# Kernel tuning notes

Hardware: AMD Instinct MI355X
Metric: run time of the kernel (lower is better)

The kernel has to match this reference:

```python
import jax, jax.numpy as jnp
import numpy as np

INPUT = 256
HIDDEN = 1024
OUTPUT = 256
B, T = 64, 512


def setup_inputs() -> dict:
    key = jax.random.key(0)
    ks = jax.random.split(key, 7)
    s_ih = 1.0 / np.sqrt(INPUT)
    s_hh = 1.0 / np.sqrt(HIDDEN)
    return {
        "input_seq": jax.random.normal(ks[0], (B, T, INPUT), jnp.float32),
        "W_ih": jax.random.uniform(ks[1], (INPUT, 4 * HIDDEN), jnp.float32, -s_ih, s_ih),
        "W_hh": jax.random.uniform(ks[2], (HIDDEN, 4 * HIDDEN), jnp.float32, -s_hh, s_hh),
        "b_ih": jax.random.uniform(ks[3], (4 * HIDDEN,), jnp.float32, -s_hh, s_hh),
        "b_hh": jax.random.uniform(ks[4], (4 * HIDDEN,), jnp.float32, -s_hh, s_hh),
        "W_out": jax.random.uniform(ks[5], (HIDDEN, OUTPUT), jnp.float32, -s_hh, s_hh),
        "b_out": jax.random.uniform(ks[6], (OUTPUT,), jnp.float32, -s_hh, s_hh),
    }


def _lstm_last_hidden(x, W_ih, W_hh, b_ih, b_hh):
    Bsz = x.shape[0]
    H = W_hh.shape[0]
    # Precompute input-side gate projections for all timesteps: [T, B, 4H]
    x_t = jnp.einsum('bti,ih->tbh', x, W_ih) + b_ih + b_hh

    def step(carry, xg):
        h, c = carry
        gates = xg + h @ W_hh  # [B, 4H]
        i, f, g, o = jnp.split(gates, 4, axis=-1)
        i = jax.nn.sigmoid(i)
        f = jax.nn.sigmoid(f)
        g = jnp.tanh(g)
        o = jax.nn.sigmoid(o)
        c = f * c + i * g
        h = o * jnp.tanh(c)
        return (h, c), None

    h0 = jnp.zeros((Bsz, H), x.dtype)
    c0 = jnp.zeros((Bsz, H), x.dtype)
    (h_last, _), _ = jax.lax.scan(step, (h0, c0), x_t)
    return h_last


def reference(input_seq, W_ih, W_hh, b_ih, b_hh, W_out, b_out):
    h_last = _lstm_last_hidden(input_seq, W_ih, W_hh, b_ih, b_hh)  # [B, H]
    return h_last @ W_out + b_out  # [B, OUTPUT]
```

## Files before the change

### kernel.cpp

```cpp
#include <hip/hip_runtime.h>
#include <hip/hip_bf16.h>
#include <cstdint>

#define HIDDEN 1024
#define INPUT  256
#define BATCH  64
#define TSTEPS 512
#define NGCOL  4096
#define KTOT   1280
#define HBUFN  65536

typedef __attribute__((ext_vector_type(8))) short bf16x8;
typedef __attribute__((ext_vector_type(4))) float f32x4;
typedef unsigned long long u64;
typedef unsigned int u32;

__device__ inline short f2bs(float f) {
    union { __hip_bfloat16 h; short s; } u;
    u.h = __float2bfloat16(f);
    return u.s;
}
__device__ inline unsigned short f2bu(float f) {
    union { __hip_bfloat16 h; unsigned short s; } u;
    u.h = __float2bfloat16(f);
    return u.s;
}

__global__ __launch_bounds__(256) void build_wt(
    const float* __restrict__ Whh, const float* __restrict__ Wih,
    __hip_bfloat16* __restrict__ Wt)
{
    int t = blockIdx.x * 256 + threadIdx.x;
    int col = t & 4095;
    int k0  = (t >> 12) * 16;
    __hip_bfloat16 tmp[16];
    if (k0 < HIDDEN) {
        #pragma unroll
        for (int i = 0; i < 16; ++i)
            tmp[i] = __float2bfloat16(Whh[(size_t)(k0 + i) * NGCOL + col]);
    } else {
        #pragma unroll
        for (int i = 0; i < 16; ++i)
            tmp[i] = __float2bfloat16(Wih[(size_t)(k0 - HIDDEN + i) * NGCOL + col]);
    }
    #pragma unroll
    for (int i = 0; i < 16; ++i)
        Wt[(size_t)col * KTOT + k0 + i] = tmp[i];
}

__global__ __launch_bounds__(256) void init_state(
    const float* __restrict__ bih, const float* __restrict__ bhh,
    float* __restrict__ bias, u32* __restrict__ hbuf)
{
    int i = blockIdx.x * 256 + threadIdx.x;
    if (i < NGCOL) bias[i] = bih[i] + bhh[i];
    hbuf[i] = 0u;
}

__global__ __launch_bounds__(512, 2) void lstm_persist(
    const __hip_bfloat16* __restrict__ Wt,
    const float* __restrict__ x,
    u32* __restrict__ hbuf,
    float* __restrict__ hf,
    const float* __restrict__ bias)
{
    __shared__ float pbuf[8][1025];

    const int tid  = threadIdx.x;
    const int wg   = blockIdx.x;
    const int bg   = wg >> 6;
    const int cg   = wg & 63;
    const int wave = tid >> 6;
    const int lane = tid & 63;
    const int l15  = lane & 15;
    const int l4   = lane >> 4;
    const int b0   = bg * 16;
    const int n0   = cg * 16;

    const __hip_bfloat16* wrow = Wt + (size_t)(n0 + l15) * KTOT;
    bf16x8 w[5][4];
    #pragma unroll
    for (int c5 = 0; c5 < 5; ++c5) {
        const int kk = (wave + c5 * 8) * 32 + l4 * 8;
        #pragma unroll
        for (int g = 0; g < 4; ++g)
            w[c5][g] = *(const bf16x8*)(wrow + (size_t)g * 1024 * KTOT + kk);
    }

    const int br = tid >> 4;
    const int hc = tid & 15;
    float creg = 0.f;
    float bi = 0.f, bfr = 0.f, bgg = 0.f, bo = 0.f;
    if (tid < 256) {
        bi  = bias[0 * 1024 + n0 + hc];
        bfr = bias[1 * 1024 + n0 + hc];
        bgg = bias[2 * 1024 + n0 + hc];
        bo  = bias[3 * 1024 + n0 + hc];
    }

    const int hoff = (b0 + l15) * HIDDEN + wave * 32 + l4 * 8;
    const float* xrow = x + ((size_t)(b0 + l15) * TSTEPS) * INPUT + wave * 32 + l4 * 8;

    for (int t = 0; t < TSTEPS; ++t) {
        const u32* hb = hbuf + (t & 1) * HBUFN;
        u32*       ho = hbuf + ((t + 1) & 1) * HBUFN;

        bf16x8 afx;
        {
            const float* xf = xrow + (size_t)t * INPUT;
            float4 pa = *(const float4*)(xf);
            float4 pb = *(const float4*)(xf + 4);
            afx[0] = f2bs(pa.x); afx[1] = f2bs(pa.y); afx[2] = f2bs(pa.z); afx[3] = f2bs(pa.w);
            afx[4] = f2bs(pb.x); afx[5] = f2bs(pb.y); afx[6] = f2bs(pb.z); afx[7] = f2bs(pb.w);
        }

        u64 hq[4][4];
        {
            const u64 want = ((u64)(u32)t << 16) | ((u64)(u32)t << 48);
            const u64 mask = 0xFFFF0000FFFF0000ull;
            for (;;) {
                u64 bad = 0;
                #pragma unroll
                for (int c5 = 0; c5 < 4; ++c5) {
                    const u64* hp = (const u64*)(hb + hoff + c5 * 256);
                    #pragma unroll
                    for (int q = 0; q < 4; ++q) {
                        hq[c5][q] = __hip_atomic_load(hp + q, __ATOMIC_RELAXED,
                                                      __HIP_MEMORY_SCOPE_AGENT);
                        bad |= (hq[c5][q] ^ want) & mask;
                    }
                }
                if (__all(bad == 0)) break;
                __builtin_amdgcn_s_sleep(1);
            }
        }
        bf16x8 afh[4];
        #pragma unroll
        for (int c5 = 0; c5 < 4; ++c5) {
            union { u32 p[4]; bf16x8 v; } u;
            #pragma unroll
            for (int q = 0; q < 4; ++q) {
                const u64 d = hq[c5][q];
                u.p[q] = (u32)(d & 0xFFFFu) | ((u32)(d >> 32) << 16);
            }
            afh[c5] = u.v;
        }

        f32x4 a0 = {0.f, 0.f, 0.f, 0.f};
        f32x4 a1 = a0, a2 = a0, a3 = a0;
        #pragma unroll
        for (int c5 = 0; c5 < 4; ++c5) {
            a0 = __builtin_amdgcn_mfma_f32_16x16x32_bf16(afh[c5], w[c5][0], a0, 0, 0, 0);
            a1 = __builtin_amdgcn_mfma_f32_16x16x32_bf16(afh[c5], w[c5][1], a1, 0, 0, 0);
            a2 = __builtin_amdgcn_mfma_f32_16x16x32_bf16(afh[c5], w[c5][2], a2, 0, 0, 0);
            a3 = __builtin_amdgcn_mfma_f32_16x16x32_bf16(afh[c5], w[c5][3], a3, 0, 0, 0);
        }
        a0 = __builtin_amdgcn_mfma_f32_16x16x32_bf16(afx, w[4][0], a0, 0, 0, 0);
        a1 = __builtin_amdgcn_mfma_f32_16x16x32_bf16(afx, w[4][1], a1, 0, 0, 0);
        a2 = __builtin_amdgcn_mfma_f32_16x16x32_bf16(afx, w[4][2], a2, 0, 0, 0);
        a3 = __builtin_amdgcn_mfma_f32_16x16x32_bf16(afx, w[4][3], a3, 0, 0, 0);

        #pragma unroll
        for (int c5 = 0; c5 < 5; ++c5)
            #pragma unroll
            for (int g = 0; g < 4; ++g)
                asm volatile("" : "+v"(w[c5][g]));

        float* pw = &pbuf[wave][0];
        #pragma unroll
        for (int r = 0; r < 4; ++r) {
            const int row = l4 * 4 + r;
            pw[(0 * 16 + row) * 16 + l15] = a0[r];
            pw[(1 * 16 + row) * 16 + l15] = a1[r];
            pw[(2 * 16 + row) * 16 + l15] = a2[r];
            pw[(3 * 16 + row) * 16 + l15] = a3[r];
        }
        __syncthreads();

        if (tid < 256) {
            float gi = bi, gf = bfr, gg = bgg, go = bo;
            #pragma unroll
            for (int w8 = 0; w8 < 8; ++w8) {
                const float* p = &pbuf[w8][0];
                gi += p[(0 * 16 + br) * 16 + hc];
                gf += p[(1 * 16 + br) * 16 + hc];
                gg += p[(2 * 16 + br) * 16 + hc];
                go += p[(3 * 16 + br) * 16 + hc];
            }
            const float i_ = 1.f / (1.f + __expf(-gi));
            const float f_ = 1.f / (1.f + __expf(-gf));
            const float g_ = tanhf(gg);
            const float o_ = 1.f / (1.f + __expf(-go));
            creg = f_ * creg + i_ * g_;
            const float h = o_ * tanhf(creg);
            if (t == TSTEPS - 1) {
                hf[(b0 + br) * HIDDEN + n0 + hc] = h;
            } else {
                const u32 val = ((u32)(t + 1) << 16) | (u32)f2bu(h);
                __hip_atomic_store(ho + (b0 + br) * HIDDEN + n0 + hc, val,
                                   __ATOMIC_RELAXED, __HIP_MEMORY_SCOPE_AGENT);
            }
        }
        if (t == TSTEPS - 1) break;
        __syncthreads();
    }
}

__global__ __launch_bounds__(256) void out_proj(
    const float* __restrict__ hf, const float* __restrict__ Wout,
    const float* __restrict__ bout, float* __restrict__ out)
{
    const int b  = blockIdx.x;
    const int oc = threadIdx.x;
    const float* hb = hf + (size_t)b * HIDDEN;
    float a0 = 0.f, a1 = 0.f, a2 = 0.f, a3 = 0.f;
    for (int k = 0; k < HIDDEN; k += 4) {
        a0 += hb[k + 0] * Wout[(size_t)(k + 0) * 256 + oc];
        a1 += hb[k + 1] * Wout[(size_t)(k + 1) * 256 + oc];
        a2 += hb[k + 2] * Wout[(size_t)(k + 2) * 256 + oc];
        a3 += hb[k + 3] * Wout[(size_t)(k + 3) * 256 + oc];
    }
    out[b * 256 + oc] = (a0 + a1) + (a2 + a3) + bout[oc];
}

extern "C" void kernel_launch(void* const* d_in, const int* in_sizes, int n_in,
                              void* d_out, int out_size, void* d_ws, size_t ws_size,
                              hipStream_t stream)
{
    const float* x    = (const float*)d_in[0];
    const float* Wih  = (const float*)d_in[1];
    const float* Whh  = (const float*)d_in[2];
    const float* bih  = (const float*)d_in[3];
    const float* bhh  = (const float*)d_in[4];
    const float* Wout = (const float*)d_in[5];
    const float* bout = (const float*)d_in[6];
    float* out = (float*)d_out;

    char* ws = (char*)d_ws;
    size_t off = 0;
    auto alloc = [&](size_t bytes) -> void* {
        void* p = ws + off;
        off = (off + bytes + 255) & ~(size_t)255;
        return p;
    };
    __hip_bfloat16* Wt = (__hip_bfloat16*)alloc((size_t)NGCOL * KTOT * 2);
    u32*   hbuf = (u32*)alloc((size_t)2 * HBUFN * 4);
    float* bias = (float*)alloc((size_t)NGCOL * 4);
    float* hf   = (float*)alloc((size_t)BATCH * HIDDEN * 4);

    build_wt<<<1280, 256, 0, stream>>>(Whh, Wih, Wt);
    init_state<<<512, 256, 0, stream>>>(bih, bhh, bias, hbuf);
    lstm_persist<<<256, 512, 0, stream>>>(Wt, x, hbuf, hf, bias);
    out_proj<<<64, 256, 0, stream>>>(hf, Wout, bout, out);
}
```

Before: 2.984 ms.

## Double-buffer LDS partials, hoist x-MFMA before spin, per-element polling

Double-buffers the per-wave partial-sum LDS array by timestep parity, so the second per-step barrier can be removed and only one raw s_barrier with an lgkmcnt wait remains. The input-projection MFMAs are moved ahead of the wait on the hidden state so they overlap the spin. The whole-wave retry loop with sleep is replaced by issuing all loads once and then re-polling each stale element individually. The aim is to shorten the serial per-step critical path, at the cost of doubled LDS use and busier polling with no sleep. The asm register pins on the weights are also dropped, which risks the compiler spilling or rematerialising them.

```diff
diff --git a/kernel.cpp b/kernel.cpp
--- a/kernel.cpp
+++ b/kernel.cpp
@@ -64,7 +64,7 @@
     float* __restrict__ hf,
     const float* __restrict__ bias)
 {
-    __shared__ float pbuf[8][1025];
+    __shared__ float pbuf[2][8][1025];
 
     const int tid  = threadIdx.x;
     const int wg   = blockIdx.x;
@@ -113,25 +113,32 @@
             afx[0] = f2bs(pa.x); afx[1] = f2bs(pa.y); afx[2] = f2bs(pa.z); afx[3] = f2bs(pa.w);
             afx[4] = f2bs(pb.x); afx[5] = f2bs(pb.y); afx[6] = f2bs(pb.z); afx[7] = f2bs(pb.w);
         }
-
+        f32x4 a0 = {0.f, 0.f, 0.f, 0.f};
+        f32x4 a1 = a0, a2 = a0, a3 = a0;
+        a0 = __builtin_amdgcn_mfma_f32_16x16x32_bf16(afx, w[4][0], a0, 0, 0, 0);
+        a1 = __builtin_amdgcn_mfma_f32_16x16x32_bf16(afx, w[4][1], a1, 0, 0, 0);
+        a2 = __builtin_amdgcn_mfma_f32_16x16x32_bf16(afx, w[4][2], a2, 0, 0, 0);
+        a3 = __builtin_amdgcn_mfma_f32_16x16x32_bf16(afx, w[4][3], a3, 0, 0, 0);
+
+        const u64 want = ((u64)(u32)t << 16) | ((u64)(u32)t << 48);
+        const u64 emask = 0xFFFF0000FFFF0000ull;
         u64 hq[4][4];
-        {
-            const u64 want = ((u64)(u32)t << 16) | ((u64)(u32)t << 48);
-            const u64 mask = 0xFFFF0000FFFF0000ull;
-            for (;;) {
-                u64 bad = 0;
-                #pragma unroll
-                for (int c5 = 0; c5 < 4; ++c5) {
-                    const u64* hp = (const u64*)(hb + hoff + c5 * 256);
-                    #pragma unroll
-                    for (int q = 0; q < 4; ++q) {
-                        hq[c5][q] = __hip_atomic_load(hp + q, __ATOMIC_RELAXED,
-                                                      __HIP_MEMORY_SCOPE_AGENT);
-                        bad |= (hq[c5][q] ^ want) & mask;
-                    }
-                }
-                if (__all(bad == 0)) break;
-                __builtin_amdgcn_s_sleep(1);
+        #pragma unroll
+        for (int c5 = 0; c5 < 4; ++c5) {
+            const u64* hp = (const u64*)(hb + hoff + c5 * 256);
+            #pragma unroll
+            for (int q = 0; q < 4; ++q)
+                hq[c5][q] = __hip_atomic_load(hp + q, __ATOMIC_RELAXED,
+                                              __HIP_MEMORY_SCOPE_AGENT);
+        }
+        #pragma unroll
+        for (int c5 = 0; c5 < 4; ++c5) {
+            const u64* hp = (const u64*)(hb + hoff + c5 * 256);
+            #pragma unroll
+            for (int q = 0; q < 4; ++q) {
+                while (((hq[c5][q] ^ want) & emask) != 0ull)
+                    hq[c5][q] = __hip_atomic_load(hp + q, __ATOMIC_RELAXED,
+                                                  __HIP_MEMORY_SCOPE_AGENT);
             }
         }
         bf16x8 afh[4];
@@ -146,8 +153,6 @@
             afh[c5] = u.v;
         }
 
-        f32x4 a0 = {0.f, 0.f, 0.f, 0.f};
-        f32x4 a1 = a0, a2 = a0, a3 = a0;
         #pragma unroll
         for (int c5 = 0; c5 < 4; ++c5) {
             a0 = __builtin_amdgcn_mfma_f32_16x16x32_bf16(afh[c5], w[c5][0], a0, 0, 0, 0);
@@ -155,18 +160,8 @@
             a2 = __builtin_amdgcn_mfma_f32_16x16x32_bf16(afh[c5], w[c5][2], a2, 0, 0, 0);
             a3 = __builtin_amdgcn_mfma_f32_16x16x32_bf16(afh[c5], w[c5][3], a3, 0, 0, 0);
         }
-        a0 = __builtin_amdgcn_mfma_f32_16x16x32_bf16(afx, w[4][0], a0, 0, 0, 0);
-        a1 = __builtin_amdgcn_mfma_f32_16x16x32_bf16(afx, w[4][1], a1, 0, 0, 0);
-        a2 = __builtin_amdgcn_mfma_f32_16x16x32_bf16(afx, w[4][2], a2, 0, 0, 0);
-        a3 = __builtin_amdgcn_mfma_f32_16x16x32_bf16(afx, w[4][3], a3, 0, 0, 0);
-
-        #pragma unroll
-        for (int c5 = 0; c5 < 5; ++c5)
-            #pragma unroll
-            for (int g = 0; g < 4; ++g)
-                asm volatile("" : "+v"(w[c5][g]));
-
-        float* pw = &pbuf[wave][0];
+
+        float* pw = &pbuf[t & 1][wave][0];
         #pragma unroll
         for (int r = 0; r < 4; ++r) {
             const int row = l4 * 4 + r;
@@ -175,13 +170,17 @@
             pw[(2 * 16 + row) * 16 + l15] = a2[r];
             pw[(3 * 16 + row) * 16 + l15] = a3[r];
         }
-        __syncthreads();
+
+        __builtin_amdgcn_sched_barrier(0);
+        asm volatile("s_waitcnt lgkmcnt(0)" ::: "memory");
+        __builtin_amdgcn_s_barrier();
+        __builtin_amdgcn_sched_barrier(0);
 
         if (tid < 256) {
             float gi = bi, gf = bfr, gg = bgg, go = bo;
             #pragma unroll
             for (int w8 = 0; w8 < 8; ++w8) {
-                const float* p = &pbuf[w8][0];
+                const float* p = &pbuf[t & 1][w8][0];
                 gi += p[(0 * 16 + br) * 16 + hc];
                 gf += p[(1 * 16 + br) * 16 + hc];
                 gg += p[(2 * 16 + br) * 16 + hc];
@@ -201,8 +200,6 @@
                                    __ATOMIC_RELAXED, __HIP_MEMORY_SCOPE_AGENT);
             }
         }
-        if (t == TSTEPS - 1) break;
-        __syncthreads();
     }
 }
 
```

New measurement: 4.193 ms. 1.41x slower.

## Stage hidden state per XCD so blocks poll XCD-local copies instead of global

Applied to the files above, without the earlier changes.

Blocks learn their XCC ID and rank through a global counter handshake. At each timestep, the waves of each XCD cooperatively copy the validated previous hidden state from the global double buffer into a per-XCD staging buffer. Each block then polls that staging copy with volatile loads, falling back to direct agent-scope atomic polling after many tries. The input-projection MFMAs are moved ahead of the wait to overlap with it. The aim is to cut cross-XCD coherent polling traffic, at the cost of an extra copy per step, a startup barrier, and reliance on volatile loads being coherent within an XCD's L2.

```diff
diff --git a/kernel.cpp b/kernel.cpp
--- a/kernel.cpp
+++ b/kernel.cpp
@@ -9,6 +9,8 @@
 #define NGCOL  4096
 #define KTOT   1280
 #define HBUFN  65536
+#define STAGEN 65536
+#define NXCD   8
 
 typedef __attribute__((ext_vector_type(8))) short bf16x8;
 typedef __attribute__((ext_vector_type(4))) float f32x4;
@@ -50,21 +52,27 @@
 
 __global__ __launch_bounds__(256) void init_state(
     const float* __restrict__ bih, const float* __restrict__ bhh,
-    float* __restrict__ bias, u32* __restrict__ hbuf)
+    float* __restrict__ bias, u32* __restrict__ hbuf,
+    u32* __restrict__ staging, u32* __restrict__ cnt)
 {
     int i = blockIdx.x * 256 + threadIdx.x;
     if (i < NGCOL) bias[i] = bih[i] + bhh[i];
-    hbuf[i] = 0u;
+    if (i < 2 * HBUFN) hbuf[i] = 0u;
+    staging[i] = 0u;
+    if (i < 256) cnt[i] = 0u;
 }
 
 __global__ __launch_bounds__(512, 2) void lstm_persist(
     const __hip_bfloat16* __restrict__ Wt,
     const float* __restrict__ x,
     u32* __restrict__ hbuf,
+    u32* __restrict__ staging,
     float* __restrict__ hf,
-    const float* __restrict__ bias)
+    const float* __restrict__ bias,
+    u32* __restrict__ cnt)
 {
     __shared__ float pbuf[8][1025];
+    __shared__ u32 pro[3];
 
     const int tid  = threadIdx.x;
     const int wg   = blockIdx.x;
@@ -77,6 +85,26 @@
     const int b0   = bg * 16;
     const int n0   = cg * 16;
 
+    if (tid == 0) {
+        u32 xcc;
+        asm volatile("s_getreg_b32 %0, hwreg(HW_REG_XCC_ID)" : "=s"(xcc));
+        xcc &= 7u;
+        u32 rank = __hip_atomic_fetch_add(cnt + xcc * 16, 1u,
+                                          __ATOMIC_RELAXED, __HIP_MEMORY_SCOPE_AGENT);
+        __hip_atomic_fetch_add(cnt + 8 * 16, 1u,
+                               __ATOMIC_RELAXED, __HIP_MEMORY_SCOPE_AGENT);
+        while (__hip_atomic_load(cnt + 8 * 16, __ATOMIC_RELAXED,
+                                 __HIP_MEMORY_SCOPE_AGENT) < 256u)
+            __builtin_amdgcn_s_sleep(2);
+        u32 nx = __hip_atomic_load(cnt + xcc * 16, __ATOMIC_RELAXED,
+                                   __HIP_MEMORY_SCOPE_AGENT);
+        pro[0] = xcc; pro[1] = rank; pro[2] = nx;
+    }
+    __syncthreads();
+    const u32 myxcd = pro[0];
+    const u32 nw    = pro[2] * 8u;
+    const u32 rw    = pro[1] * 8u + (u32)wave;
+
     const __hip_bfloat16* wrow = Wt + (size_t)(n0 + l15) * KTOT;
     bf16x8 w[5][4];
     #pragma unroll
@@ -104,34 +132,72 @@
     for (int t = 0; t < TSTEPS; ++t) {
         const u32* hb = hbuf + (t & 1) * HBUFN;
         u32*       ho = hbuf + ((t + 1) & 1) * HBUFN;
+        u32*       sg = staging + ((size_t)myxcd * 2 + (t & 1)) * STAGEN;
+
+        const u64 want  = ((u64)(u32)t << 16) | ((u64)(u32)t << 48);
+        const u64 emask = 0xFFFF0000FFFF0000ull;
+
+        const float* xf = xrow + (size_t)t * INPUT;
+        float4 pa = *(const float4*)(xf);
+        float4 pb = *(const float4*)(xf + 4);
+
+        for (u32 s = rw; s < 256u; s += nw) {
+            const u32 off = (s >> 2) * 1024u + (s & 3u) * 256u + (u32)lane * 4u;
+            const u64* sp = (const u64*)(hb + off);
+            u64 d0, d1;
+            for (;;) {
+                d0 = __hip_atomic_load(sp,     __ATOMIC_RELAXED, __HIP_MEMORY_SCOPE_AGENT);
+                d1 = __hip_atomic_load(sp + 1, __ATOMIC_RELAXED, __HIP_MEMORY_SCOPE_AGENT);
+                if (__all((((d0 ^ want) | (d1 ^ want)) & emask) == 0ull)) break;
+                __builtin_amdgcn_s_sleep(1);
+            }
+            u64* dp = (u64*)(sg + off);
+            dp[0] = d0; dp[1] = d1;
+        }
 
         bf16x8 afx;
-        {
-            const float* xf = xrow + (size_t)t * INPUT;
-            float4 pa = *(const float4*)(xf);
-            float4 pb = *(const float4*)(xf + 4);
-            afx[0] = f2bs(pa.x); afx[1] = f2bs(pa.y); afx[2] = f2bs(pa.z); afx[3] = f2bs(pa.w);
-            afx[4] = f2bs(pb.x); afx[5] = f2bs(pb.y); afx[6] = f2bs(pb.z); afx[7] = f2bs(pb.w);
-        }
+        afx[0] = f2bs(pa.x); afx[1] = f2bs(pa.y); afx[2] = f2bs(pa.z); afx[3] = f2bs(pa.w);
+        afx[4] = f2bs(pb.x); afx[5] = f2bs(pb.y); afx[6] = f2bs(pb.z); afx[7] = f2bs(pb.w);
+        f32x4 a0 = {0.f, 0.f, 0.f, 0.f};
+        f32x4 a1 = a0, a2 = a0, a3 = a0;
+        a0 = __builtin_amdgcn_mfma_f32_16x16x32_bf16(afx, w[4][0], a0, 0, 0, 0);
+        a1 = __builtin_amdgcn_mfma_f32_16x16x32_bf16(afx, w[4][1], a1, 0, 0, 0);
+        a2 = __builtin_amdgcn_mfma_f32_16x16x32_bf16(afx, w[4][2], a2, 0, 0, 0);
+        a3 = __builtin_amdgcn_mfma_f32_16x16x32_bf16(afx, w[4][3], a3, 0, 0, 0);
 
         u64 hq[4][4];
         {
-            const u64 want = ((u64)(u32)t << 16) | ((u64)(u32)t << 48);
-            const u64 mask = 0xFFFF0000FFFF0000ull;
-            for (;;) {
+            int tries = 0; bool ok = false;
+            while (!ok) {
                 u64 bad = 0;
                 #pragma unroll
                 for (int c5 = 0; c5 < 4; ++c5) {
-                    const u64* hp = (const u64*)(hb + hoff + c5 * 256);
+                    volatile const u64* vp = (volatile const u64*)(sg + hoff + c5 * 256);
                     #pragma unroll
                     for (int q = 0; q < 4; ++q) {
-                        hq[c5][q] = __hip_atomic_load(hp + q, __ATOMIC_RELAXED,
-                                                      __HIP_MEMORY_SCOPE_AGENT);
-                        bad |= (hq[c5][q] ^ want) & mask;
+                        hq[c5][q] = vp[q];
+                        bad |= (hq[c5][q] ^ want) & emask;
                     }
                 }
-                if (__all(bad == 0)) break;
-                __builtin_amdgcn_s_sleep(1);
+                ok = __all(bad == 0);
+                if (!ok && ++tries > 2048) break;
+            }
+            if (!ok) {
+                for (;;) {
+                    u64 bad = 0;
+                    #pragma unroll
+                    for (int c5 = 0; c5 < 4; ++c5) {
+                        const u64* hp = (const u64*)(hb + hoff + c5 * 256);
+                        #pragma unroll
+                        for (int q = 0; q < 4; ++q) {
+                            hq[c5][q] = __hip_atomic_load(hp + q, __ATOMIC_RELAXED,
+                                                          __HIP_MEMORY_SCOPE_AGENT);
+                            bad |= (hq[c5][q] ^ want) & emask;
+                        }
+                    }
+                    if (__all(bad == 0)) break;
+                    __builtin_amdgcn_s_sleep(1);
+                }
             }
         }
         bf16x8 afh[4];
@@ -146,8 +212,6 @@
             afh[c5] = u.v;
         }
 
-        f32x4 a0 = {0.f, 0.f, 0.f, 0.f};
-        f32x4 a1 = a0, a2 = a0, a3 = a0;
         #pragma unroll
         for (int c5 = 0; c5 < 4; ++c5) {
             a0 = __builtin_amdgcn_mfma_f32_16x16x32_bf16(afh[c5], w[c5][0], a0, 0, 0, 0);
@@ -155,16 +219,6 @@
             a2 = __builtin_amdgcn_mfma_f32_16x16x32_bf16(afh[c5], w[c5][2], a2, 0, 0, 0);
             a3 = __builtin_amdgcn_mfma_f32_16x16x32_bf16(afh[c5], w[c5][3], a3, 0, 0, 0);
         }
-        a0 = __builtin_amdgcn_mfma_f32_16x16x32_bf16(afx, w[4][0], a0, 0, 0, 0);
-        a1 = __builtin_amdgcn_mfma_f32_16x16x32_bf16(afx, w[4][1], a1, 0, 0, 0);
-        a2 = __builtin_amdgcn_mfma_f32_16x16x32_bf16(afx, w[4][2], a2, 0, 0, 0);
-        a3 = __builtin_amdgcn_mfma_f32_16x16x32_bf16(afx, w[4][3], a3, 0, 0, 0);
-
-        #pragma unroll
-        for (int c5 = 0; c5 < 5; ++c5)
-            #pragma unroll
-            for (int g = 0; g < 4; ++g)
-                asm volatile("" : "+v"(w[c5][g]));
 
         float* pw = &pbuf[wave][0];
         #pragma unroll
@@ -244,12 +298,14 @@
         return p;
     };
     __hip_bfloat16* Wt = (__hip_bfloat16*)alloc((size_t)NGCOL * KTOT * 2);
-    u32*   hbuf = (u32*)alloc((size_t)2 * HBUFN * 4);
-    float* bias = (float*)alloc((size_t)NGCOL * 4);
-    float* hf   = (float*)alloc((size_t)BATCH * HIDDEN * 4);
+    u32*   hbuf    = (u32*)alloc((size_t)2 * HBUFN * 4);
+    u32*   staging = (u32*)alloc((size_t)NXCD * 2 * STAGEN * 4);
+    float* bias    = (float*)alloc((size_t)NGCOL * 4);
+    float* hf      = (float*)alloc((size_t)BATCH * HIDDEN * 4);
+    u32*   cnt     = (u32*)alloc((size_t)256 * 4);
 
     build_wt<<<1280, 256, 0, stream>>>(Whh, Wih, Wt);
-    init_state<<<512, 256, 0, stream>>>(bih, bhh, bias, hbuf);
-    lstm_persist<<<256, 512, 0, stream>>>(Wt, x, hbuf, hf, bias);
+    init_state<<<4096, 256, 0, stream>>>(bih, bhh, bias, hbuf, staging, cnt);
+    lstm_persist<<<256, 512, 0, stream>>>(Wt, x, hbuf, staging, hf, bias, cnt);
     out_proj<<<64, 256, 0, stream>>>(hf, Wout, bout, out);
 }
```

Measured after the change: 4.917 ms. 1.65x slower.

## Poll per-producer sentinels and hoist input MFMAs before the h-state wait

Applied to the files above, without the earlier changes.

Each lane now polls one sentinel word per producer column group instead of spinning on the full 16-word hidden-state read, then does a single full load with fallback retries. The input-projection MFMAs are issued before the wait so they overlap the barrier latency. Column-group assignment is remapped across blocks, presumably to spread producers across XCDs or caches. This cuts polling traffic on the critical per-step barrier, but relies on the sentinel ordering matching the producers' write pattern. The empty asm statements that pinned the weights in registers are also removed.

```diff
diff --git a/kernel.cpp b/kernel.cpp
--- a/kernel.cpp
+++ b/kernel.cpp
@@ -67,9 +67,9 @@
     __shared__ float pbuf[8][1025];
 
     const int tid  = threadIdx.x;
-    const int wg   = blockIdx.x;
-    const int bg   = wg >> 6;
-    const int cg   = wg & 63;
+    const int i    = blockIdx.x;
+    const int cg   = (i & 7) * 8 + ((i >> 3) & 7);
+    const int bg   = i >> 6;
     const int wave = tid >> 6;
     const int lane = tid & 63;
     const int l15  = lane & 15;
@@ -101,6 +101,11 @@
     const int hoff = (b0 + l15) * HIDDEN + wave * 32 + l4 * 8;
     const float* xrow = x + ((size_t)(b0 + l15) * TSTEPS) * INPUT + wave * 32 + l4 * 8;
 
+    const int jj  = lane & 7;
+    const int rr  = (lane >> 3) & 3;
+    const int pcg = 2 * wave + (jj & 1) + 16 * ((jj >> 1) & 3);
+    const int sentoff = (b0 + 4 * rr + 3) * HIDDEN + pcg * 16 + ((lane >= 32) ? 7 : 15);
+
     for (int t = 0; t < TSTEPS; ++t) {
         const u32* hb = hbuf + (t & 1) * HBUFN;
         u32*       ho = hbuf + ((t + 1) & 1) * HBUFN;
@@ -113,13 +118,41 @@
             afx[0] = f2bs(pa.x); afx[1] = f2bs(pa.y); afx[2] = f2bs(pa.z); afx[3] = f2bs(pa.w);
             afx[4] = f2bs(pb.x); afx[5] = f2bs(pb.y); afx[6] = f2bs(pb.z); afx[7] = f2bs(pb.w);
         }
-
+        f32x4 a0 = {0.f, 0.f, 0.f, 0.f};
+        f32x4 a1 = a0, a2 = a0, a3 = a0;
+        a0 = __builtin_amdgcn_mfma_f32_16x16x32_bf16(afx, w[4][0], a0, 0, 0, 0);
+        a1 = __builtin_amdgcn_mfma_f32_16x16x32_bf16(afx, w[4][1], a1, 0, 0, 0);
+        a2 = __builtin_amdgcn_mfma_f32_16x16x32_bf16(afx, w[4][2], a2, 0, 0, 0);
+        a3 = __builtin_amdgcn_mfma_f32_16x16x32_bf16(afx, w[4][3], a3, 0, 0, 0);
+
+        {
+            const u32 wantu = (u32)t << 16;
+            for (;;) {
+                u32 v = __hip_atomic_load(hb + sentoff, __ATOMIC_RELAXED,
+                                          __HIP_MEMORY_SCOPE_AGENT);
+                if (__all(((v ^ wantu) & 0xFFFF0000u) == 0)) break;
+                __builtin_amdgcn_s_sleep(1);
+            }
+        }
+
+        const u64 want  = ((u64)(u32)t << 16) | ((u64)(u32)t << 48);
+        const u64 emask = 0xFFFF0000FFFF0000ull;
         u64 hq[4][4];
         {
-            const u64 want = ((u64)(u32)t << 16) | ((u64)(u32)t << 48);
-            const u64 mask = 0xFFFF0000FFFF0000ull;
-            for (;;) {
-                u64 bad = 0;
+            u64 bad = 0;
+            #pragma unroll
+            for (int c5 = 0; c5 < 4; ++c5) {
+                const u64* hp = (const u64*)(hb + hoff + c5 * 256);
+                #pragma unroll
+                for (int q = 0; q < 4; ++q) {
+                    hq[c5][q] = __hip_atomic_load(hp + q, __ATOMIC_RELAXED,
+                                                  __HIP_MEMORY_SCOPE_AGENT);
+                    bad |= (hq[c5][q] ^ want) & emask;
+                }
+            }
+            while (!__all(bad == 0)) {
+                __builtin_amdgcn_s_sleep(1);
+                bad = 0;
                 #pragma unroll
                 for (int c5 = 0; c5 < 4; ++c5) {
                     const u64* hp = (const u64*)(hb + hoff + c5 * 256);
@@ -127,11 +160,9 @@
                     for (int q = 0; q < 4; ++q) {
                         hq[c5][q] = __hip_atomic_load(hp + q, __ATOMIC_RELAXED,
                                                       __HIP_MEMORY_SCOPE_AGENT);
-                        bad |= (hq[c5][q] ^ want) & mask;
+                        bad |= (hq[c5][q] ^ want) & emask;
                     }
                 }
-                if (__all(bad == 0)) break;
-                __builtin_amdgcn_s_sleep(1);
             }
         }
         bf16x8 afh[4];
@@ -146,8 +177,6 @@
             afh[c5] = u.v;
         }
 
-        f32x4 a0 = {0.f, 0.f, 0.f, 0.f};
-        f32x4 a1 = a0, a2 = a0, a3 = a0;
         #pragma unroll
         for (int c5 = 0; c5 < 4; ++c5) {
             a0 = __builtin_amdgcn_mfma_f32_16x16x32_bf16(afh[c5], w[c5][0], a0, 0, 0, 0);
@@ -155,16 +184,6 @@
             a2 = __builtin_amdgcn_mfma_f32_16x16x32_bf16(afh[c5], w[c5][2], a2, 0, 0, 0);
             a3 = __builtin_amdgcn_mfma_f32_16x16x32_bf16(afh[c5], w[c5][3], a3, 0, 0, 0);
         }
-        a0 = __builtin_amdgcn_mfma_f32_16x16x32_bf16(afx, w[4][0], a0, 0, 0, 0);
-        a1 = __builtin_amdgcn_mfma_f32_16x16x32_bf16(afx, w[4][1], a1, 0, 0, 0);
-        a2 = __builtin_amdgcn_mfma_f32_16x16x32_bf16(afx, w[4][2], a2, 0, 0, 0);
-        a3 = __builtin_amdgcn_mfma_f32_16x16x32_bf16(afx, w[4][3], a3, 0, 0, 0);
-
-        #pragma unroll
-        for (int c5 = 0; c5 < 5; ++c5)
-            #pragma unroll
-            for (int g = 0; g < 4; ++g)
-                asm volatile("" : "+v"(w[c5][g]));
 
         float* pw = &pbuf[wave][0];
         #pragma unroll
```

Result: no change. 2.973 ms (-0.4%).
